# Kernel optimization log

Hardware: AMD Instinct MI355X
Metric: run time of the kernel (lower is better)

## Reference

```python
import jax, jax.numpy as jnp
import numpy as np

N_SPK = 2048
M_UTT = 8
D_EMB = 512


def setup_inputs() -> dict:
    key = jax.random.key(0)
    k1, = jax.random.split(key, 1)
    embeds = jax.random.normal(k1, (N_SPK * M_UTT, D_EMB), dtype=jnp.float32)
    # module expects L2-normalized utterance embeddings
    embeds = embeds / jnp.linalg.norm(embeds, axis=-1, keepdims=True)
    return {
        "embeds": embeds,
        "w": jnp.asarray(10.0, dtype=jnp.float32),
        "b": jnp.asarray(-5.0, dtype=jnp.float32),
        "n_speakers": N_SPK,
        "m_utterances": M_UTT,
    }


def reference(embeds, w, b, n_speakers, m_utterances):
    N, M = n_speakers, m_utterances
    D = embeds.shape[-1]
    e = embeds.reshape(N, M, D)

    # full centroids (all M utterances), L2-normalized
    centroids = e.mean(axis=1)  # [N, D]
    centroids = centroids / jnp.linalg.norm(centroids, axis=-1, keepdims=True)

    # leave-one-out centroids for same-speaker comparisons
    sums = e.sum(axis=1, keepdims=True)  # [N, 1, D]
    excl = (sums - e) / (M - 1)  # [N, M, D]
    excl = excl / jnp.linalg.norm(excl, axis=-1, keepdims=True)

    # similarity: batched GEMM replaces the original triple loop
    sim = jnp.einsum("nmd,kd->nmk", e, centroids)  # [N, M, N]
    # diagonal (k == i) uses leave-one-out centroid
    diag = jnp.sum(e * excl, axis=-1)  # [N, M]
    idx = jnp.arange(N)
    sim = sim.at[idx, :, idx].set(diag)

    sim = jnp.abs(w) * sim + b

    # cross-entropy with label = own speaker index
    logits = sim.reshape(N * M, N)
    labels = jnp.repeat(jnp.arange(N), M)
    logp = jax.nn.log_softmax(logits, axis=-1)
    loss = -jnp.mean(logp[jnp.arange(N * M), labels])
    return loss
```

## Files before the change

kernel.cpp:

```cpp
#include <hip/hip_runtime.h>
#include <hip/hip_bf16.h>
#include <string.h>

#define N_SPK 2048
#define M_UTT 8
#define D_EMB 512
#define N_ROWS (N_SPK * M_UTT)

using short8 = __attribute__((ext_vector_type(8))) short;
using f32x4  = __attribute__((ext_vector_type(4))) float;

typedef const __attribute__((address_space(1))) unsigned int* gas_p;
typedef __attribute__((address_space(3))) unsigned int* las_p;

__device__ int            g_flag;
__device__ float          g_diag[N_ROWS];
__device__ unsigned short g_cRow[N_SPK * D_EMB];
__device__ float          g_rowsum[N_ROWS * 4];

__device__ __forceinline__ float u2f(unsigned int u) { float f; memcpy(&f, &u, 4); return f; }
__device__ __forceinline__ unsigned int f2u(float f) { unsigned int u; memcpy(&u, &f, 4); return u; }
__device__ __forceinline__ float bflo(unsigned int u) { return u2f(u << 16); }
__device__ __forceinline__ float bfhi(unsigned int u) { return u2f(u & 0xFFFF0000u); }
__device__ __forceinline__ unsigned short f2bf(float f) {
    unsigned int u = f2u(f);
    unsigned int r = u + 0x7FFFu + ((u >> 16) & 1u);
    return (unsigned short)(r >> 16);
}
__device__ __forceinline__ float wsum(float v) {
#pragma unroll
    for (int off = 32; off > 0; off >>= 1) v += __shfl_xor(v, off, 64);
    return v;
}
__device__ __forceinline__ float loadScalar(const void* p, int isbf) {
    float vb = bflo((unsigned int)(*(const unsigned short*)p));
    float vf = *(const float*)p;
    float prim = isbf ? vb : vf;
    float alt  = isbf ? vf : vb;
    float a = fabsf(prim);
    if (isfinite(prim) && a > 1e-6f && a < 1e6f) return prim;
    return alt;
}
__device__ __forceinline__ short8 loadA8(const void* e, long row, int d0, int isbf) {
    if (isbf) {
        return *(const short8*)((const unsigned short*)e + row * D_EMB + d0);
    } else {
        const float* q = (const float*)e + row * D_EMB + d0;
        short8 r;
#pragma unroll
        for (int j = 0; j < 8; ++j) r[j] = (short)f2bf(q[j]);
        return r;
    }
}
__device__ __forceinline__ int detectWave(const void* e, long row, int lane) {
    const unsigned short* q = (const unsigned short*)e + row * D_EMB + lane * 8;
    float p = 0.f;
#pragma unroll
    for (int j = 0; j < 8; ++j) {
        float v = bflo((unsigned int)q[j]);
        p += v * v;
    }
    p = wsum(p);
    return (fabsf(p - 1.0f) < 0.25f) ? 1 : 0;
}

__global__ __launch_bounds__(256) void k1_cent(const void* e) {
    int t = threadIdx.x;
    int wave = t >> 6, lane = t & 63;
    int n = blockIdx.x * 4 + wave;

    int isbf = detectWave(e, (long)n * M_UTT, lane);
    if (blockIdx.x == 0 && t == 0) g_flag = isbf;

    float ev[M_UTT][8];
    size_t base = (size_t)n * (M_UTT * D_EMB);
#pragma unroll
    for (int m = 0; m < M_UTT; ++m) {
        size_t idx = base + (size_t)m * D_EMB + (size_t)lane * 8;
        if (isbf) {
            uint4 v = *(const uint4*)((const unsigned short*)e + idx);
            ev[m][0] = bflo(v.x); ev[m][1] = bfhi(v.x);
            ev[m][2] = bflo(v.y); ev[m][3] = bfhi(v.y);
            ev[m][4] = bflo(v.z); ev[m][5] = bfhi(v.z);
            ev[m][6] = bflo(v.w); ev[m][7] = bfhi(v.w);
        } else {
            const float* q = (const float*)e + idx;
            float4 a = *(const float4*)q;
            float4 b2 = *(const float4*)(q + 4);
            ev[m][0] = a.x; ev[m][1] = a.y; ev[m][2] = a.z; ev[m][3] = a.w;
            ev[m][4] = b2.x; ev[m][5] = b2.y; ev[m][6] = b2.z; ev[m][7] = b2.w;
        }
    }

    float s[8];
#pragma unroll
    for (int j = 0; j < 8; ++j) {
        float acc = 0.f;
#pragma unroll
        for (int m = 0; m < M_UTT; ++m) acc += ev[m][j];
        s[j] = acc;
    }

    float p = 0.f;
#pragma unroll
    for (int j = 0; j < 8; ++j) p += s[j] * s[j];
    p = wsum(p);
    float inv = rsqrtf(p);

    unsigned short cw[8];
#pragma unroll
    for (int j = 0; j < 8; ++j) cw[j] = f2bf(s[j] * inv);
    *(short8*)&g_cRow[(size_t)n * D_EMB + lane * 8] = *(short8*)cw;

#pragma unroll
    for (int m = 0; m < M_UTT; ++m) {
        float pd = 0.f, pn = 0.f;
#pragma unroll
        for (int j = 0; j < 8; ++j) {
            float ex = s[j] - ev[m][j];
            pd += ev[m][j] * ex;
            pn += ex * ex;
        }
        pd = wsum(pd);
        pn = wsum(pn);
        if (lane == 0) g_diag[n * M_UTT + m] = pd * rsqrtf(pn);
    }
}

__global__ __launch_bounds__(256, 2) void GE2ELoss_70626442215524_kernel(
        const void* e, const void* wp, const void* bp) {
    __shared__ unsigned short sB[2][16 * 512];

    int t = threadIdx.x;
    int wave = t >> 6, lane = t & 63;
    int bx = blockIdx.x;
    int rowgrp = bx >> 2, qtr = bx & 3;
    int rowbase = rowgrp * 128 + wave * 32;
    int isbf = g_flag;
    int quad = lane >> 4, l16 = lane & 15;

    float w_ = fabsf(loadScalar(wp, isbf));
    float b_ = loadScalar(bp, isbf);

    {
        int c0 = qtr * 512;
#pragma unroll
        for (int i = 0; i < 4; ++i) {
            int cb = i * 256 + wave * 64;
            int w = cb + lane;
            int row = w & 15;
            int dc = ((w >> 6) << 2) + ((w >> 4) & 3);
            const unsigned short* g = &g_cRow[((size_t)(c0 + row) << 9) + dc * 8];
            __builtin_amdgcn_global_load_lds((gas_p)g, (las_p)&sB[0][cb * 8], 16, 0, 0);
        }
    }

    short8 a[2][16];
#pragma unroll
    for (int s = 0; s < 2; ++s) {
        long row = rowbase + s * 16 + l16;
#pragma unroll
        for (int kt = 0; kt < 16; ++kt)
            a[s][kt] = loadA8(e, row, kt * 32 + quad * 8, isbf);
    }

    float rsum[2][4];
#pragma unroll
    for (int s = 0; s < 2; ++s)
#pragma unroll
        for (int r = 0; r < 4; ++r) rsum[s][r] = 0.f;

    __syncthreads();

    for (int nt = 0; nt < 32; ++nt) {
        int cur = nt & 1;

        if (nt + 1 < 32) {
            int c0n = (qtr * 32 + nt + 1) * 16;
#pragma unroll
            for (int i = 0; i < 4; ++i) {
                int cb = i * 256 + wave * 64;
                int w = cb + lane;
                int row = w & 15;
                int dc = ((w >> 6) << 2) + ((w >> 4) & 3);
                const unsigned short* g = &g_cRow[((size_t)(c0n + row) << 9) + dc * 8];
                __builtin_amdgcn_global_load_lds((gas_p)g, (las_p)&sB[cur ^ 1][cb * 8], 16, 0, 0);
            }
        }

        f32x4 acc0 = {0.f, 0.f, 0.f, 0.f}, acc1 = {0.f, 0.f, 0.f, 0.f};
#pragma unroll
        for (int kt = 0; kt < 16; ++kt) {
            short8 b = *(const short8*)&sB[cur][(kt * 64 + lane) * 8];
            acc0 = __builtin_amdgcn_mfma_f32_16x16x32_bf16(a[0][kt], b, acc0, 0, 0, 0);
            acc1 = __builtin_amdgcn_mfma_f32_16x16x32_bf16(a[1][kt], b, acc1, 0, 0, 0);
        }

        int gcol = (qtr * 32 + nt) * 16 + l16;
#pragma unroll
        for (int s = 0; s < 2; ++s) {
            f32x4 acc = s ? acc1 : acc0;
#pragma unroll
            for (int reg = 0; reg < 4; ++reg) {
                int grow = rowbase + s * 16 + quad * 4 + reg;
                float v = fmaf(w_, acc[reg], b_);
                if (gcol == (grow >> 3)) v = fmaf(w_, g_diag[grow], b_);
                rsum[s][reg] += __expf(v);
            }
        }

        __syncthreads();
    }

#pragma unroll
    for (int s = 0; s < 2; ++s)
#pragma unroll
        for (int reg = 0; reg < 4; ++reg) {
            float v = rsum[s][reg];
            v += __shfl_xor(v, 1, 64);
            v += __shfl_xor(v, 2, 64);
            v += __shfl_xor(v, 4, 64);
            v += __shfl_xor(v, 8, 64);
            if (l16 == 0) {
                int grow = rowbase + s * 16 + quad * 4 + reg;
                g_rowsum[grow * 4 + qtr] = v;
            }
        }
}

__global__ void k3_fin(const void* wp, const void* bp, unsigned int* out) {
    __shared__ float red[1024];
    int t = threadIdx.x;
    int isbf = g_flag;
    float w_ = fabsf(loadScalar(wp, isbf));
    float b_ = loadScalar(bp, isbf);

    float s = 0.f;
    for (int r = t; r < N_ROWS; r += 1024) {
        float tot = g_rowsum[r * 4] + g_rowsum[r * 4 + 1] + g_rowsum[r * 4 + 2] + g_rowsum[r * 4 + 3];
        s += logf(tot) - fmaf(w_, g_diag[r], b_);
    }
    red[t] = s;
    __syncthreads();
    for (int off = 512; off > 0; off >>= 1) {
        if (t < off) red[t] += red[t + off];
        __syncthreads();
    }
    if (t == 0) {
        float loss = red[0] * (1.0f / N_ROWS);
        unsigned int h = (unsigned int)f2bf(loss);
        out[0] = (h << 16) | h;
    }
}

extern "C" void kernel_launch(void* const* d_in, const int* in_sizes, int n_in,
                              void* d_out, int out_size, void* d_ws, size_t ws_size,
                              hipStream_t stream) {
    const void* e  = d_in[0];
    const void* wp = d_in[1];
    const void* bp = d_in[2];
    (void)in_sizes; (void)n_in; (void)out_size; (void)d_ws; (void)ws_size;

    k1_cent<<<512, 256, 0, stream>>>(e);
    GE2ELoss_70626442215524_kernel<<<512, 256, 0, stream>>>(e, wp, bp);
    k3_fin<<<1, 1024, 0, stream>>>(wp, bp, (unsigned int*)d_out);
}
```

Before: 140.1 us.

## Widen GEMM column tile to 32, reorder block mapping, parallelize final reduction

The main GEMM kernel now stages two 16-column centroid tiles per iteration, halving the number of loop iterations and barriers and giving more independent MFMA chains per step, at the cost of twice the LDS (64KB per block). The block index mapping is changed so consecutive blocks share the same column quarter, which may improve L2 reuse of centroid tiles. The single-block final reduction is replaced by 64 blocks that use wave shuffles and atomic accumulation, with a last-block-done counter writing the loss. The extra LDS may lower occupancy, and the atomic float sum makes the result order nondeterministic.

Measured after the change: 136.0 us. -3.0%, faster.

```diff
diff --git a/kernel.cpp b/kernel.cpp
--- a/kernel.cpp
+++ b/kernel.cpp
@@ -14,6 +14,8 @@
 typedef __attribute__((address_space(3))) unsigned int* las_p;
 
 __device__ int            g_flag;
+__device__ float          g_accum;
+__device__ unsigned int   g_done;
 __device__ float          g_diag[N_ROWS];
 __device__ unsigned short g_cRow[N_SPK * D_EMB];
 __device__ float          g_rowsum[N_ROWS * 4];
@@ -70,7 +72,7 @@
     int n = blockIdx.x * 4 + wave;
 
     int isbf = detectWave(e, (long)n * M_UTT, lane);
-    if (blockIdx.x == 0 && t == 0) g_flag = isbf;
+    if (blockIdx.x == 0 && t == 0) { g_flag = isbf; g_accum = 0.f; g_done = 0u; }
 
     float ev[M_UTT][8];
     size_t base = (size_t)n * (M_UTT * D_EMB);
@@ -129,12 +131,12 @@
 
 __global__ __launch_bounds__(256, 2) void GE2ELoss_70626442215524_kernel(
         const void* e, const void* wp, const void* bp) {
-    __shared__ unsigned short sB[2][16 * 512];
+    __shared__ unsigned short sB[2][2][16 * 512];
 
     int t = threadIdx.x;
     int wave = t >> 6, lane = t & 63;
     int bx = blockIdx.x;
-    int rowgrp = bx >> 2, qtr = bx & 3;
+    int qtr = bx >> 7, rowgrp = bx & 127;
     int rowbase = rowgrp * 128 + wave * 32;
     int isbf = g_flag;
     int quad = lane >> 4, l16 = lane & 15;
@@ -142,70 +144,69 @@
     float w_ = fabsf(loadScalar(wp, isbf));
     float b_ = loadScalar(bp, isbf);
 
-    {
-        int c0 = qtr * 512;
-#pragma unroll
-        for (int i = 0; i < 4; ++i) {
-            int cb = i * 256 + wave * 64;
-            int w = cb + lane;
-            int row = w & 15;
-            int dc = ((w >> 6) << 2) + ((w >> 4) & 3);
-            const unsigned short* g = &g_cRow[((size_t)(c0 + row) << 9) + dc * 8];
-            __builtin_amdgcn_global_load_lds((gas_p)g, (las_p)&sB[0][cb * 8], 16, 0, 0);
-        }
-    }
-
-    short8 a[2][16];
-#pragma unroll
-    for (int s = 0; s < 2; ++s) {
-        long row = rowbase + s * 16 + l16;
-#pragma unroll
-        for (int kt = 0; kt < 16; ++kt)
-            a[s][kt] = loadA8(e, row, kt * 32 + quad * 8, isbf);
-    }
-
-    float rsum[2][4];
-#pragma unroll
-    for (int s = 0; s < 2; ++s)
-#pragma unroll
-        for (int r = 0; r < 4; ++r) rsum[s][r] = 0.f;
-
-    __syncthreads();
-
-    for (int nt = 0; nt < 32; ++nt) {
-        int cur = nt & 1;
-
-        if (nt + 1 < 32) {
-            int c0n = (qtr * 32 + nt + 1) * 16;
+    auto stageTile = [&](int buf, int nt2) {
+        int c0 = qtr * 512 + nt2 * 32;
+#pragma unroll
+        for (int g = 0; g < 2; ++g) {
 #pragma unroll
             for (int i = 0; i < 4; ++i) {
                 int cb = i * 256 + wave * 64;
                 int w = cb + lane;
-                int row = w & 15;
+                int col = w & 15;
                 int dc = ((w >> 6) << 2) + ((w >> 4) & 3);
-                const unsigned short* g = &g_cRow[((size_t)(c0n + row) << 9) + dc * 8];
-                __builtin_amdgcn_global_load_lds((gas_p)g, (las_p)&sB[cur ^ 1][cb * 8], 16, 0, 0);
-            }
-        }
-
-        f32x4 acc0 = {0.f, 0.f, 0.f, 0.f}, acc1 = {0.f, 0.f, 0.f, 0.f};
-#pragma unroll
-        for (int kt = 0; kt < 16; ++kt) {
-            short8 b = *(const short8*)&sB[cur][(kt * 64 + lane) * 8];
-            acc0 = __builtin_amdgcn_mfma_f32_16x16x32_bf16(a[0][kt], b, acc0, 0, 0, 0);
-            acc1 = __builtin_amdgcn_mfma_f32_16x16x32_bf16(a[1][kt], b, acc1, 0, 0, 0);
-        }
-
-        int gcol = (qtr * 32 + nt) * 16 + l16;
-#pragma unroll
-        for (int s = 0; s < 2; ++s) {
-            f32x4 acc = s ? acc1 : acc0;
-#pragma unroll
-            for (int reg = 0; reg < 4; ++reg) {
-                int grow = rowbase + s * 16 + quad * 4 + reg;
-                float v = fmaf(w_, acc[reg], b_);
-                if (gcol == (grow >> 3)) v = fmaf(w_, g_diag[grow], b_);
-                rsum[s][reg] += __expf(v);
+                const unsigned short* g_ = &g_cRow[((size_t)(c0 + g * 16 + col) << 9) + dc * 8];
+                __builtin_amdgcn_global_load_lds((gas_p)g_, (las_p)&sB[buf][g][cb * 8], 16, 0, 0);
+            }
+        }
+    };
+
+    stageTile(0, 0);
+
+    short8 a[2][16];
+#pragma unroll
+    for (int s = 0; s < 2; ++s) {
+        long row = rowbase + s * 16 + l16;
+#pragma unroll
+        for (int kt = 0; kt < 16; ++kt)
+            a[s][kt] = loadA8(e, row, kt * 32 + quad * 8, isbf);
+    }
+
+    float rsum[2][4];
+#pragma unroll
+    for (int s = 0; s < 2; ++s)
+#pragma unroll
+        for (int r = 0; r < 4; ++r) rsum[s][r] = 0.f;
+
+    __syncthreads();
+
+    for (int nt2 = 0; nt2 < 16; ++nt2) {
+        int cur = nt2 & 1;
+        if (nt2 + 1 < 16) stageTile(cur ^ 1, nt2 + 1);
+
+        f32x4 acc[2][2] = {{{0.f,0.f,0.f,0.f},{0.f,0.f,0.f,0.f}},
+                           {{0.f,0.f,0.f,0.f},{0.f,0.f,0.f,0.f}}};
+#pragma unroll
+        for (int g = 0; g < 2; ++g) {
+#pragma unroll
+            for (int kt = 0; kt < 16; ++kt) {
+                short8 b = *(const short8*)&sB[cur][g][(kt * 64 + lane) * 8];
+                acc[g][0] = __builtin_amdgcn_mfma_f32_16x16x32_bf16(a[0][kt], b, acc[g][0], 0, 0, 0);
+                acc[g][1] = __builtin_amdgcn_mfma_f32_16x16x32_bf16(a[1][kt], b, acc[g][1], 0, 0, 0);
+            }
+        }
+
+#pragma unroll
+        for (int g = 0; g < 2; ++g) {
+            int gcol = qtr * 512 + nt2 * 32 + g * 16 + l16;
+#pragma unroll
+            for (int s = 0; s < 2; ++s) {
+#pragma unroll
+                for (int reg = 0; reg < 4; ++reg) {
+                    int grow = rowbase + s * 16 + quad * 4 + reg;
+                    float v = fmaf(w_, acc[g][s][reg], b_);
+                    if (gcol == (grow >> 3)) v = fmaf(w_, g_diag[grow], b_);
+                    rsum[s][reg] += __expf(v);
+                }
             }
         }
 
@@ -228,28 +229,31 @@
         }
 }
 
-__global__ void k3_fin(const void* wp, const void* bp, unsigned int* out) {
-    __shared__ float red[1024];
-    int t = threadIdx.x;
+__global__ __launch_bounds__(256) void k3_fin(const void* wp, const void* bp, unsigned int* out) {
+    __shared__ float red[4];
+    int t = threadIdx.x, bx = blockIdx.x;
     int isbf = g_flag;
     float w_ = fabsf(loadScalar(wp, isbf));
     float b_ = loadScalar(bp, isbf);
 
-    float s = 0.f;
-    for (int r = t; r < N_ROWS; r += 1024) {
-        float tot = g_rowsum[r * 4] + g_rowsum[r * 4 + 1] + g_rowsum[r * 4 + 2] + g_rowsum[r * 4 + 3];
-        s += logf(tot) - fmaf(w_, g_diag[r], b_);
-    }
-    red[t] = s;
+    int r = bx * 256 + t;
+    float4 q = *(const float4*)&g_rowsum[r * 4];
+    float tot = (q.x + q.y) + (q.z + q.w);
+    float s = logf(tot) - fmaf(w_, g_diag[r], b_);
+
+    s = wsum(s);
+    if ((t & 63) == 0) red[t >> 6] = s;
     __syncthreads();
-    for (int off = 512; off > 0; off >>= 1) {
-        if (t < off) red[t] += red[t + off];
-        __syncthreads();
-    }
     if (t == 0) {
-        float loss = red[0] * (1.0f / N_ROWS);
-        unsigned int h = (unsigned int)f2bf(loss);
-        out[0] = (h << 16) | h;
+        float part = red[0] + red[1] + red[2] + red[3];
+        atomicAdd(&g_accum, part);
+        __threadfence();
+        unsigned int old = atomicAdd(&g_done, 1u);
+        if (old == 63u) {
+            float loss = atomicAdd(&g_accum, 0.f) * (1.0f / N_ROWS);
+            unsigned int h = (unsigned int)f2bf(loss);
+            out[0] = (h << 16) | h;
+        }
     }
 }
 
@@ -263,5 +267,5 @@
 
     k1_cent<<<512, 256, 0, stream>>>(e);
     GE2ELoss_70626442215524_kernel<<<512, 256, 0, stream>>>(e, wp, bp);
-    k3_fin<<<1, 1024, 0, stream>>>(wp, bp, (unsigned int*)d_out);
-}
+    k3_fin<<<64, 256, 0, stream>>>(wp, bp, (unsigned int*)d_out);
+}
```

## Enlarge GEMM row tile to 64 rows per wave and fuse final reduction

Applied to the files above, without the earlier changes.

Each wave now handles 64 rows (4 MFMA row tiles) instead of 32, so every staged centroid tile in LDS is reused across twice as many rows and the grid halves to 256 blocks. Block order is changed so blocks sharing a centroid quarter are adjacent. The separate final-loss kernel is removed: the last block to finish, found with an atomic counter, computes the log-sum and mean, which saves one launch. The cost is higher register pressure (occupancy hint drops to 1), fewer blocks to hide latency, and a serial tail reduction inside one block.

Measured after the change: 200.5 us. 43.1% more time.

```diff
diff --git a/kernel.cpp b/kernel.cpp
--- a/kernel.cpp
+++ b/kernel.cpp
@@ -14,6 +14,7 @@
 typedef __attribute__((address_space(3))) unsigned int* las_p;
 
 __device__ int            g_flag;
+__device__ unsigned int   g_done;
 __device__ float          g_diag[N_ROWS];
 __device__ unsigned short g_cRow[N_SPK * D_EMB];
 __device__ float          g_rowsum[N_ROWS * 4];
@@ -70,7 +71,7 @@
     int n = blockIdx.x * 4 + wave;
 
     int isbf = detectWave(e, (long)n * M_UTT, lane);
-    if (blockIdx.x == 0 && t == 0) g_flag = isbf;
+    if (blockIdx.x == 0 && t == 0) { g_flag = isbf; g_done = 0u; }
 
     float ev[M_UTT][8];
     size_t base = (size_t)n * (M_UTT * D_EMB);
@@ -127,46 +128,49 @@
     }
 }
 
-__global__ __launch_bounds__(256, 2) void GE2ELoss_70626442215524_kernel(
-        const void* e, const void* wp, const void* bp) {
+__global__ __launch_bounds__(256, 1) void GE2ELoss_70626442215524_kernel(
+        const void* e, const void* wp, const void* bp, unsigned int* out) {
     __shared__ unsigned short sB[2][16 * 512];
+    __shared__ float fred[256];
+    __shared__ int lastflag;
 
     int t = threadIdx.x;
     int wave = t >> 6, lane = t & 63;
     int bx = blockIdx.x;
-    int rowgrp = bx >> 2, qtr = bx & 3;
-    int rowbase = rowgrp * 128 + wave * 32;
+    int qtr = bx >> 6, rowgrp = bx & 63;
+    int rowbase = rowgrp * 256 + wave * 64;
     int isbf = g_flag;
     int quad = lane >> 4, l16 = lane & 15;
 
     float w_ = fabsf(loadScalar(wp, isbf));
     float b_ = loadScalar(bp, isbf);
 
-    {
-        int c0 = qtr * 512;
+    auto stageTile = [&](int buf, int nt) {
+        int c0 = qtr * 512 + nt * 16;
 #pragma unroll
         for (int i = 0; i < 4; ++i) {
-            int cb = i * 256 + wave * 64;
-            int w = cb + lane;
-            int row = w & 15;
+            int w = t + i * 256;
+            int col = w & 15;
             int dc = ((w >> 6) << 2) + ((w >> 4) & 3);
-            const unsigned short* g = &g_cRow[((size_t)(c0 + row) << 9) + dc * 8];
-            __builtin_amdgcn_global_load_lds((gas_p)g, (las_p)&sB[0][cb * 8], 16, 0, 0);
-        }
-    }
-
-    short8 a[2][16];
-#pragma unroll
-    for (int s = 0; s < 2; ++s) {
+            const unsigned short* g_ = &g_cRow[((size_t)(c0 + col) << 9) + dc * 8];
+            __builtin_amdgcn_global_load_lds((gas_p)g_, (las_p)&sB[buf][(size_t)w * 8], 16, 0, 0);
+        }
+    };
+
+    stageTile(0, 0);
+
+    short8 a[4][16];
+#pragma unroll
+    for (int s = 0; s < 4; ++s) {
         long row = rowbase + s * 16 + l16;
 #pragma unroll
         for (int kt = 0; kt < 16; ++kt)
             a[s][kt] = loadA8(e, row, kt * 32 + quad * 8, isbf);
     }
 
-    float rsum[2][4];
-#pragma unroll
-    for (int s = 0; s < 2; ++s)
+    float rsum[4][4];
+#pragma unroll
+    for (int s = 0; s < 4; ++s)
 #pragma unroll
         for (int r = 0; r < 4; ++r) rsum[s][r] = 0.f;
 
@@ -174,36 +178,25 @@
 
     for (int nt = 0; nt < 32; ++nt) {
         int cur = nt & 1;
-
-        if (nt + 1 < 32) {
-            int c0n = (qtr * 32 + nt + 1) * 16;
-#pragma unroll
-            for (int i = 0; i < 4; ++i) {
-                int cb = i * 256 + wave * 64;
-                int w = cb + lane;
-                int row = w & 15;
-                int dc = ((w >> 6) << 2) + ((w >> 4) & 3);
-                const unsigned short* g = &g_cRow[((size_t)(c0n + row) << 9) + dc * 8];
-                __builtin_amdgcn_global_load_lds((gas_p)g, (las_p)&sB[cur ^ 1][cb * 8], 16, 0, 0);
-            }
-        }
-
-        f32x4 acc0 = {0.f, 0.f, 0.f, 0.f}, acc1 = {0.f, 0.f, 0.f, 0.f};
+        if (nt + 1 < 32) stageTile(cur ^ 1, nt + 1);
+
+        f32x4 acc[4] = {{0.f,0.f,0.f,0.f},{0.f,0.f,0.f,0.f},
+                        {0.f,0.f,0.f,0.f},{0.f,0.f,0.f,0.f}};
 #pragma unroll
         for (int kt = 0; kt < 16; ++kt) {
             short8 b = *(const short8*)&sB[cur][(kt * 64 + lane) * 8];
-            acc0 = __builtin_amdgcn_mfma_f32_16x16x32_bf16(a[0][kt], b, acc0, 0, 0, 0);
-            acc1 = __builtin_amdgcn_mfma_f32_16x16x32_bf16(a[1][kt], b, acc1, 0, 0, 0);
-        }
-
-        int gcol = (qtr * 32 + nt) * 16 + l16;
-#pragma unroll
-        for (int s = 0; s < 2; ++s) {
-            f32x4 acc = s ? acc1 : acc0;
+#pragma unroll
+            for (int s = 0; s < 4; ++s)
+                acc[s] = __builtin_amdgcn_mfma_f32_16x16x32_bf16(a[s][kt], b, acc[s], 0, 0, 0);
+        }
+
+        int gcol = qtr * 512 + nt * 16 + l16;
+#pragma unroll
+        for (int s = 0; s < 4; ++s) {
 #pragma unroll
             for (int reg = 0; reg < 4; ++reg) {
                 int grow = rowbase + s * 16 + quad * 4 + reg;
-                float v = fmaf(w_, acc[reg], b_);
+                float v = fmaf(w_, acc[s][reg], b_);
                 if (gcol == (grow >> 3)) v = fmaf(w_, g_diag[grow], b_);
                 rsum[s][reg] += __expf(v);
             }
@@ -213,7 +206,7 @@
     }
 
 #pragma unroll
-    for (int s = 0; s < 2; ++s)
+    for (int s = 0; s < 4; ++s)
 #pragma unroll
         for (int reg = 0; reg < 4; ++reg) {
             float v = rsum[s][reg];
@@ -226,28 +219,30 @@
                 g_rowsum[grow * 4 + qtr] = v;
             }
         }
-}
-
-__global__ void k3_fin(const void* wp, const void* bp, unsigned int* out) {
-    __shared__ float red[1024];
-    int t = threadIdx.x;
-    int isbf = g_flag;
-    float w_ = fabsf(loadScalar(wp, isbf));
-    float b_ = loadScalar(bp, isbf);
+
+    __syncthreads();
+    if (t == 0) {
+        __threadfence();
+        unsigned int old = atomicAdd(&g_done, 1u);
+        lastflag = (old == 255u);
+    }
+    __syncthreads();
+    if (!lastflag) return;
 
     float s = 0.f;
-    for (int r = t; r < N_ROWS; r += 1024) {
-        float tot = g_rowsum[r * 4] + g_rowsum[r * 4 + 1] + g_rowsum[r * 4 + 2] + g_rowsum[r * 4 + 3];
+    for (int r = t; r < N_ROWS; r += 256) {
+        float4 q = *(const float4*)&g_rowsum[r * 4];
+        float tot = (q.x + q.y) + (q.z + q.w);
         s += logf(tot) - fmaf(w_, g_diag[r], b_);
     }
-    red[t] = s;
-    __syncthreads();
-    for (int off = 512; off > 0; off >>= 1) {
-        if (t < off) red[t] += red[t + off];
+    fred[t] = s;
+    __syncthreads();
+    for (int off = 128; off > 0; off >>= 1) {
+        if (t < off) fred[t] += fred[t + off];
         __syncthreads();
     }
     if (t == 0) {
-        float loss = red[0] * (1.0f / N_ROWS);
+        float loss = fred[0] * (1.0f / N_ROWS);
         unsigned int h = (unsigned int)f2bf(loss);
         out[0] = (h << 16) | h;
     }
@@ -262,6 +257,5 @@
     (void)in_sizes; (void)n_in; (void)out_size; (void)d_ws; (void)ws_size;
 
     k1_cent<<<512, 256, 0, stream>>>(e);
-    GE2ELoss_70626442215524_kernel<<<512, 256, 0, stream>>>(e, wp, bp);
-    k3_fin<<<1, 1024, 0, stream>>>(wp, bp, (unsigned int*)d_out);
-}
+    GE2ELoss_70626442215524_kernel<<<256, 256, 0, stream>>>(e, wp, bp, (unsigned int*)d_out);
+}
```
